# Optimization experiments

Hardware: AMD Instinct MI355X
Metric: run time of the kernel (lower is better)

Reference implementation:

```python
import jax, jax.numpy as jnp
import numpy as np

POSE, Z, H, E = 62, 32, 256, 6

def setup_inputs() -> dict:
    key = jax.random.key(0)
    ks = jax.random.split(key, 32)
    it = iter(ks)
    def W(o, i):
        return (jax.random.normal(next(it), (o, i), jnp.float32) * 0.05)
    def B(o):
        return jnp.zeros((o,), jnp.float32)
    def WE(o, i):
        return (jax.random.normal(next(it), (E, o, i), jnp.float32) * 0.05)
    def BE(o):
        return jnp.zeros((E, o), jnp.float32)
    d = {}
    d['prev_pose'] = jax.random.normal(next(it), (POSE,), jnp.float32)
    d['curr_pose'] = jax.random.normal(next(it), (POSE,), jnp.float32)
    d['eps'] = jax.random.normal(next(it), (Z,), jnp.float32)
    # encoder
    d['enc_w0'], d['enc_b0'] = W(H, POSE + POSE), B(H)
    d['enc_w1'], d['enc_b1'] = W(H, H), B(H)
    d['enc_w2'], d['enc_b2'] = W(H, H), B(H)
    d['mu_w'], d['mu_b'] = W(Z, H), B(Z)
    d['lv_w'], d['lv_b'] = W(Z, H), B(Z)
    # gating network
    d['gate_w0'], d['gate_b0'] = W(H, Z + POSE), B(H)
    d['gate_w1'], d['gate_b1'] = W(H, H), B(H)
    d['gate_w2'], d['gate_b2'] = W(H, H), B(H)
    d['gate_w3'], d['gate_b3'] = W(E, H), B(E)
    # 6 experts, stacked on leading expert axis
    d['exp_w0'], d['exp_b0'] = WE(H, Z + POSE), BE(H)
    d['exp_w1'], d['exp_b1'] = WE(H, Z + H), BE(H)
    d['exp_w2'], d['exp_b2'] = WE(H, Z + H), BE(H)
    d['exp_w3'], d['exp_b3'] = WE(POSE, Z + H), BE(POSE)
    return d

def _forward(prev_pose, curr_pose, eps,
             enc_w0, enc_b0, enc_w1, enc_b1, enc_w2, enc_b2,
             mu_w, mu_b, lv_w, lv_b,
             gate_w0, gate_b0, gate_w1, gate_b1, gate_w2, gate_b2,
             gate_w3, gate_b3,
             exp_w0, exp_b0, exp_w1, exp_b1, exp_w2, exp_b2,
             exp_w3, exp_b3):
    elu = jax.nn.elu
    # encode
    x = elu(enc_w0 @ jnp.concatenate([prev_pose, curr_pose]) + enc_b0)
    x = elu(enc_w1 @ x + enc_b1)
    x = elu(enc_w2 @ x + enc_b2)
    mu = mu_w @ x + mu_b
    logvar = lv_w @ x + lv_b
    # reparameterize (eps supplied as input for determinism)
    z = mu + eps * jnp.exp(0.5 * logvar)
    # gating network (raw logits, no softmax -- as in the original)
    g_in = jnp.concatenate([z, prev_pose])  # [94]
    g = elu(gate_w0 @ g_in + gate_b0)
    g = elu(gate_w1 @ g + gate_b1)
    g = elu(gate_w2 @ g + gate_b2)
    gates = gate_w3 @ g + gate_b3  # [6]
    # all 6 experts batched along leading axis e
    z_e = jnp.broadcast_to(z, (E, Z))  # [6,32]
    h = elu(jnp.einsum('eoh,h->eo', exp_w0, g_in) + exp_b0)       # [6,256]
    h = elu(jnp.einsum('eoh,eh->eo', exp_w1,
                       jnp.concatenate([z_e, h], axis=1)) + exp_b1)
    h = elu(jnp.einsum('eoh,eh->eo', exp_w2,
                       jnp.concatenate([z_e, h], axis=1)) + exp_b2)
    out_e = jnp.einsum('eoh,eh->eo', exp_w3,
                       jnp.concatenate([z_e, h], axis=1)) + exp_b3  # [6,62]
    decoded = jnp.sum(out_e * gates[:, None], axis=0)  # [62]
    return decoded, mu, logvar

def reference(prev_pose, curr_pose, eps,
              enc_w0, enc_b0, enc_w1, enc_b1, enc_w2, enc_b2,
              mu_w, mu_b, lv_w, lv_b,
              gate_w0, gate_b0, gate_w1, gate_b1, gate_w2, gate_b2,
              gate_w3, gate_b3,
              exp_w0, exp_b0, exp_w1, exp_b1, exp_w2, exp_b2,
              exp_w3, exp_b3):
    return _forward(prev_pose, curr_pose, eps,
                    enc_w0, enc_b0, enc_w1, enc_b1, enc_w2, enc_b2,
                    mu_w, mu_b, lv_w, lv_b,
                    gate_w0, gate_b0, gate_w1, gate_b1, gate_w2, gate_b2,
                    gate_w3, gate_b3,
                    exp_w0, exp_b0, exp_w1, exp_b1, exp_w2, exp_b2,
                    exp_w3, exp_b3)
```

## Files before the change

kernel.cpp:

```cpp
#include <hip/hip_runtime.h>
#include <math.h>


#define NWG    128
#define NWAVES (NWG * 4)
#define BLOCK  256
#define MAGIC  0x7E57A11E

__device__ __align__(128) float g_a0[256];
__device__ __align__(128) float g_a1[256];
__device__ __align__(128) float g_a2[256];
__device__ __align__(128) float g_mu[32];
__device__ __align__(128) float g_lv[32];
__device__ __align__(128) float g_g0[256];
__device__ __align__(128) float g_g1[256];
__device__ __align__(128) float g_g2[256];
__device__ __align__(128) float g_gates[32];
__device__ __align__(128) float g_h0[1536];
__device__ __align__(128) float g_h1[1536];
__device__ __align__(128) float g_h2[1536];
__device__ __align__(128) float g_oute[384];

struct P {
  const float *prev, *curr, *eps;
  const float *ew0,*eb0,*ew1,*eb1,*ew2,*eb2;
  const float *muw,*mub,*lvw,*lvb;
  const float *gw0,*gb0,*gw1,*gb1,*gw2,*gb2,*gw3,*gb3;
  const float *xw0,*xb0,*xw1,*xb1,*xw2,*xb2,*xw3,*xb3;
  float* out;
};

__device__ __forceinline__ float cload(const float* a) {
  int v = __hip_atomic_load((const int*)a, __ATOMIC_RELAXED,
                            __HIP_MEMORY_SCOPE_AGENT);
  return __int_as_float(v);
}
__device__ __forceinline__ void cstore(float* a, float v) {
  __hip_atomic_store((int*)a, __float_as_int(v), __ATOMIC_RELAXED,
                     __HIP_MEMORY_SCOPE_AGENT);
}
__device__ __forceinline__ float4 cload4(const float* a) {
  float4 r;
  r.x = cload(a + 0); r.y = cload(a + 1);
  r.z = cload(a + 2); r.w = cload(a + 3);
  return r;
}
__device__ __forceinline__ void gll16(const void* g, void* l) {
  __builtin_amdgcn_global_load_lds((const __attribute__((address_space(1))) void*)g,
                                   (__attribute__((address_space(3))) void*)l,
                                   16, 0, 0);
}
__device__ __forceinline__ void gll4(const void* g, void* l) {
  __builtin_amdgcn_global_load_lds((const __attribute__((address_space(1))) void*)g,
                                   (__attribute__((address_space(3))) void*)l,
                                   4, 0, 0);
}
__device__ __forceinline__ float wred(float v) {
#pragma unroll
  for (int m = 32; m; m >>= 1) v += __shfl_xor(v, m, 64);
  return v;
}
__device__ __forceinline__ float elu(float x) { return x > 0.f ? x : expm1f(x); }
__device__ __forceinline__ float dot4(float4 a, float4 b) {
  return a.x*b.x + a.y*b.y + a.z*b.z + a.w*b.w;
}

__device__ __forceinline__ int* slotp(int* flags, int ph, int wg) {
  return &flags[((ph - 1) * NWG + wg) * 16];
}
__device__ __forceinline__ void bar_arrive(int* flags, int ph) {
  __syncthreads();
  if (threadIdx.x == 0)
    __hip_atomic_store(slotp(flags, ph, blockIdx.x), MAGIC,
                       __ATOMIC_RELAXED, __HIP_MEMORY_SCOPE_AGENT);
}
__device__ __forceinline__ void bar_poll(int* flags, int ph, int nprod) {
  if (threadIdx.x < 64) {
    const int l = threadIdx.x;
    for (;;) {
      bool ok = true;
      for (int w = l; w < nprod; w += 64)
        ok &= (__hip_atomic_load(slotp(flags, ph, w),
                                 __ATOMIC_RELAXED, __HIP_MEMORY_SCOPE_AGENT)
               == MAGIC);
      if (ok) break;
      __builtin_amdgcn_s_sleep(2);
    }
  }
  __syncthreads();
}

__global__ __launch_bounds__(BLOCK, 1) void mvae_main(P p, int* flags) {
  const int tid  = threadIdx.x;
  const int lane = tid & 63;
  const int wvin = tid >> 6;
  const int Wv   = blockIdx.x * 4 + wvin;

  __shared__ __align__(16) float s_w1[4][256];
  __shared__ __align__(16) float s_w2[4][256];
  __shared__ __align__(16) float s_w3[4][256];
  __shared__ __align__(16) float s_w4[4][4][96];
  __shared__ __align__(16) float s_w5[4][4][288];
  __shared__ __align__(16) float s_w6[4][4][288];
  __shared__ __align__(16) float s_w7[4][288];
  __shared__ float s_o[384];
  __shared__ float s_gg[8];

  if (Wv < 256)
    gll16(p.ew1 + Wv * 256 + lane * 4, s_w1[wvin]);

  if (Wv < 256) {
    const float* wr = p.ew0 + Wv * 124;
    float wa = wr[lane];
    float wb = (lane < 60) ? wr[64 + lane] : 0.f;
    float xa = (lane < 62) ? p.prev[lane] : p.curr[lane - 62];
    float xb = (lane < 60) ? p.curr[lane + 2] : 0.f;
    float s = wred(wa * xa + wb * xb);
    if (!lane) cstore(&g_a0[Wv], elu(s + p.eb0[Wv]));
  }
  bar_arrive(flags, 1);
  if (Wv < 256)
    gll16(p.ew2 + Wv * 256 + lane * 4, s_w2[wvin]);
  if (Wv < 64) {
    const float* src = (Wv < 32) ? p.muw + Wv * 256 : p.lvw + (Wv - 32) * 256;
    gll16(src + lane * 4, s_w3[wvin]);
  }
  bar_poll(flags, 1, 64);

  if (Wv < 256) {
    float4 w = *(const float4*)(s_w1[wvin] + 4 * lane);
    float4 x = cload4(g_a0 + 4 * lane);
    float s = wred(dot4(w, x));
    if (!lane) cstore(&g_a1[Wv], elu(s + p.eb1[Wv]));
  }
  bar_arrive(flags, 2);
#pragma unroll
  for (int k = 0; k < 4; ++k) {
    int r = Wv + NWAVES * k;
    if (r < 1792) {
      const float* src = (r < 256) ? p.gw0 + r * 94 : p.xw0 + (size_t)(r - 256) * 94;
      float* dst = s_w4[wvin][k];
      if (lane < 23)       gll16(src + lane * 4, dst);
      else if (lane == 23) { gll4(src + 92, dst + 69);
                             gll4(src + 93, dst + 70); }
    }
  }
#pragma unroll
  for (int k = 0; k < 4; ++k) {
    int r = Wv + NWAVES * k;
    if (r < 1792) {
      float* dst = s_w5[wvin][k];
      if (r < 256) gll16(p.gw1 + r * 256 + lane * 4, dst);
      else {
        const float* src = p.xw1 + (size_t)(r - 256) * 288;
        gll16(src + lane * 4, dst);
        if (lane < 8) gll16(src + 256 + lane * 4, dst + 256);
      }
    }
  }
  bar_poll(flags, 2, 64);

  if (Wv < 256) {
    float4 w = *(const float4*)(s_w2[wvin] + 4 * lane);
    float4 x = cload4(g_a1 + 4 * lane);
    float s = wred(dot4(w, x));
    if (!lane) cstore(&g_a2[Wv], elu(s + p.eb2[Wv]));
  }
  bar_arrive(flags, 3);
#pragma unroll
  for (int k = 0; k < 4; ++k) {
    int r = Wv + NWAVES * k;
    if (r < 1792) {
      float* dst = s_w6[wvin][k];
      if (r < 256) gll16(p.gw2 + r * 256 + lane * 4, dst);
      else {
        const float* src = p.xw2 + (size_t)(r - 256) * 288;
        gll16(src + lane * 4, dst);
        if (lane < 8) gll16(src + 256 + lane * 4, dst + 256);
      }
    }
  }
  if (Wv < 6) {
    gll16(p.gw3 + Wv * 256 + lane * 4, s_w7[wvin]);
  } else if (Wv < 378) {
    const float* src = p.xw3 + (size_t)(Wv - 6) * 288;
    float* dst = s_w7[wvin];
    gll16(src + lane * 4, dst);
    if (lane < 8) gll16(src + 256 + lane * 4, dst + 256);
  }
  bar_poll(flags, 3, 64);

  if (Wv < 64) {
    float4 w = *(const float4*)(s_w3[wvin] + 4 * lane);
    float4 x = cload4(g_a2 + 4 * lane);
    float s = wred(dot4(w, x));
    if (!lane) {
      if (Wv < 32) { float v = s + p.mub[Wv]; cstore(&g_mu[Wv], v); p.out[62 + Wv] = v; }
      else { int r = Wv - 32; float v = s + p.lvb[r]; cstore(&g_lv[r], v); p.out[94 + r] = v; }
    }
  }
  bar_arrive(flags, 4);
  bar_poll(flags, 4, 16);

  float zs = 0.f;
  if (lane < 32)
    zs = cload(&g_mu[lane]) + p.eps[lane] * expf(0.5f * cload(&g_lv[lane]));
  float4 z4;
  z4.x = __shfl(zs, (4 * lane + 0) & 63, 64);
  z4.y = __shfl(zs, (4 * lane + 1) & 63, 64);
  z4.z = __shfl(zs, (4 * lane + 2) & 63, 64);
  z4.w = __shfl(zs, (4 * lane + 3) & 63, 64);
  float prevA = (lane >= 32 && lane < 94) ? p.prev[lane - 32] : 0.f;
  float prevB = (lane < 30) ? p.prev[32 + lane] : 0.f;
  float xa94 = (lane < 32) ? zs : prevA;

#pragma unroll
  for (int k = 0; k < 4; ++k) {
    int r = Wv + NWAVES * k;
    if (r < 1792) {
      const float* wrow = s_w4[wvin][k];
      float wa = wrow[lane];
      float wb = (lane < 30) ? wrow[64 + lane] : 0.f;
      float s = wred(wa * xa94 + wb * prevB);
      if (!lane) {
        if (r < 256) cstore(&g_g0[r], elu(s + p.gb0[r]));
        else         cstore(&g_h0[r - 256], elu(s + p.xb0[r - 256]));
      }
    }
  }
  bar_arrive(flags, 5);
  bar_poll(flags, 5, NWG);

#pragma unroll
  for (int k = 0; k < 4; ++k) {
    int r = Wv + NWAVES * k;
    if (r < 1792) {
      const float* wrow = s_w5[wvin][k];
      float4 w = *(const float4*)(wrow + 4 * lane);
      if (r < 256) {
        float4 x = cload4(g_g0 + 4 * lane);
        float s = wred(dot4(w, x));
        if (!lane) cstore(&g_g1[r], elu(s + p.gb1[r]));
      } else {
        int q = r - 256, e = q >> 8;
        const float* hsrc = g_h0 + e * 256;
        float4 xh = z4;
        if (lane >= 8) xh = cload4(hsrc + 4 * lane - 32);
        float s = dot4(w, xh);
        if (lane < 32) s += wrow[256 + lane] * cload(hsrc + 224 + lane);
        s = wred(s);
        if (!lane) cstore(&g_h1[q], elu(s + p.xb1[q]));
      }
    }
  }
  bar_arrive(flags, 6);
  bar_poll(flags, 6, NWG);

#pragma unroll
  for (int k = 0; k < 4; ++k) {
    int r = Wv + NWAVES * k;
    if (r < 1792) {
      const float* wrow = s_w6[wvin][k];
      float4 w = *(const float4*)(wrow + 4 * lane);
      if (r < 256) {
        float4 x = cload4(g_g1 + 4 * lane);
        float s = wred(dot4(w, x));
        if (!lane) cstore(&g_g2[r], elu(s + p.gb2[r]));
      } else {
        int q = r - 256, e = q >> 8;
        const float* hsrc = g_h1 + e * 256;
        float4 xh = z4;
        if (lane >= 8) xh = cload4(hsrc + 4 * lane - 32);
        float s = dot4(w, xh);
        if (lane < 32) s += wrow[256 + lane] * cload(hsrc + 224 + lane);
        s = wred(s);
        if (!lane) cstore(&g_h2[q], elu(s + p.xb2[q]));
      }
    }
  }
  bar_arrive(flags, 7);
  bar_poll(flags, 7, NWG);

  if (Wv < 6) {
    float4 w = *(const float4*)(s_w7[wvin] + 4 * lane);
    float4 x = cload4(g_g2 + 4 * lane);
    float s = wred(dot4(w, x));
    if (!lane) cstore(&g_gates[Wv], s + p.gb3[Wv]);
  } else if (Wv < 378) {
    int q = Wv - 6, e = q / 62;
    const float* wrow = s_w7[wvin];
    float4 w = *(const float4*)(wrow + 4 * lane);
    const float* hsrc = g_h2 + e * 256;
    float4 xh = z4;
    if (lane >= 8) xh = cload4(hsrc + 4 * lane - 32);
    float s = dot4(w, xh);
    if (lane < 32) s += wrow[256 + lane] * cload(hsrc + 224 + lane);
    s = wred(s);
    if (!lane) cstore(&g_oute[q], s + p.xb3[q]);
  }

  bar_arrive(flags, 8);
  if (blockIdx.x != 0) return;
  bar_poll(flags, 8, NWG);

  s_o[tid] = cload(&g_oute[tid]);
  if (tid < 116) s_o[tid + 256] = cload(&g_oute[tid + 256]);
  if (tid < 6)   s_gg[tid] = cload(&g_gates[tid]);
  __syncthreads();
  if (tid < 62) {
    float s = 0.f;
#pragma unroll
    for (int e = 0; e < 6; ++e) s += s_o[e * 62 + tid] * s_gg[e];
    p.out[tid] = s;
  }

  for (int idx = tid; idx < 8 * NWG; idx += BLOCK)
    __hip_atomic_store(&flags[idx * 16], 0,
                       __ATOMIC_RELAXED, __HIP_MEMORY_SCOPE_AGENT);
}

extern "C" void kernel_launch(void* const* d_in, const int* in_sizes, int n_in,
                              void* d_out, int out_size, void* d_ws, size_t ws_size,
                              hipStream_t stream) {
  (void)in_sizes; (void)n_in; (void)out_size; (void)ws_size;
  const float* const* in = (const float* const*)d_in;
  P p;
  p.prev = in[0];  p.curr = in[1];  p.eps = in[2];
  p.ew0 = in[3];   p.eb0 = in[4];   p.ew1 = in[5];  p.eb1 = in[6];
  p.ew2 = in[7];   p.eb2 = in[8];
  p.muw = in[9];   p.mub = in[10];  p.lvw = in[11]; p.lvb = in[12];
  p.gw0 = in[13];  p.gb0 = in[14];  p.gw1 = in[15]; p.gb1 = in[16];
  p.gw2 = in[17];  p.gb2 = in[18];  p.gw3 = in[19]; p.gb3 = in[20];
  p.xw0 = in[21];  p.xb0 = in[22];  p.xw1 = in[23]; p.xb1 = in[24];
  p.xw2 = in[25];  p.xb2 = in[26];  p.xw3 = in[27]; p.xb3 = in[28];
  p.out = (float*)d_out;

  int* flags = (int*)d_ws;
  mvae_main<<<NWG, BLOCK, 0, stream>>>(p, flags);
}
```

Measured before the change: 33.08 us.

## Compute mu/logvar redundantly per block to remove a grid barrier

Every block now loads all 64 mu/logvar weight rows into LDS and computes mu, logvar and z locally. This removes the grid-wide barrier phase that used to publish those values through global memory. Blocks outside the first 64 also skip polling phases 1 and 2, since they produce nothing for those phases, and the poll sleep interval is shortened. The cost is 64KB of extra LDS per block and redundant weight traffic and compute in all 128 blocks.

```diff
diff --git a/kernel.cpp b/kernel.cpp
--- a/kernel.cpp
+++ b/kernel.cpp
@@ -6,12 +6,11 @@
 #define NWAVES (NWG * 4)
 #define BLOCK  256
 #define MAGIC  0x7E57A11E
+#define NPHASE 7
 
 __device__ __align__(128) float g_a0[256];
 __device__ __align__(128) float g_a1[256];
 __device__ __align__(128) float g_a2[256];
-__device__ __align__(128) float g_mu[32];
-__device__ __align__(128) float g_lv[32];
 __device__ __align__(128) float g_g0[256];
 __device__ __align__(128) float g_g1[256];
 __device__ __align__(128) float g_g2[256];
@@ -84,7 +83,7 @@
                                  __ATOMIC_RELAXED, __HIP_MEMORY_SCOPE_AGENT)
                == MAGIC);
       if (ok) break;
-      __builtin_amdgcn_s_sleep(2);
+      __builtin_amdgcn_s_sleep(1);
     }
   }
   __syncthreads();
@@ -95,14 +94,17 @@
   const int lane = tid & 63;
   const int wvin = tid >> 6;
   const int Wv   = blockIdx.x * 4 + wvin;
+  const bool early = (blockIdx.x < 64);
 
   __shared__ __align__(16) float s_w1[4][256];
   __shared__ __align__(16) float s_w2[4][256];
-  __shared__ __align__(16) float s_w3[4][256];
+  __shared__ __align__(16) float s_wml[4][16 * 256];
   __shared__ __align__(16) float s_w4[4][4][96];
   __shared__ __align__(16) float s_w5[4][4][288];
   __shared__ __align__(16) float s_w6[4][4][288];
   __shared__ __align__(16) float s_w7[4][288];
+  __shared__ float s_ml[64];
+  __shared__ float s_z[32];
   __shared__ float s_o[384];
   __shared__ float s_gg[8];
 
@@ -121,11 +123,14 @@
   bar_arrive(flags, 1);
   if (Wv < 256)
     gll16(p.ew2 + Wv * 256 + lane * 4, s_w2[wvin]);
-  if (Wv < 64) {
-    const float* src = (Wv < 32) ? p.muw + Wv * 256 : p.lvw + (Wv - 32) * 256;
-    gll16(src + lane * 4, s_w3[wvin]);
-  }
-  bar_poll(flags, 1, 64);
+#pragma unroll
+  for (int i = 0; i < 16; ++i) {
+    int row = wvin * 16 + i;
+    const float* src = (row < 32) ? p.muw + row * 256
+                                  : p.lvw + (row - 32) * 256;
+    gll16(src + lane * 4, s_wml[wvin] + i * 256);
+  }
+  if (early) bar_poll(flags, 1, 64);
 
   if (Wv < 256) {
     float4 w = *(const float4*)(s_w1[wvin] + 4 * lane);
@@ -158,7 +163,7 @@
       }
     }
   }
-  bar_poll(flags, 2, 64);
+  if (early) bar_poll(flags, 2, 64);
 
   if (Wv < 256) {
     float4 w = *(const float4*)(s_w2[wvin] + 4 * lane);
@@ -190,29 +195,28 @@
   }
   bar_poll(flags, 3, 64);
 
-  if (Wv < 64) {
-    float4 w = *(const float4*)(s_w3[wvin] + 4 * lane);
+  {
     float4 x = cload4(g_a2 + 4 * lane);
-    float s = wred(dot4(w, x));
-    if (!lane) {
-      if (Wv < 32) { float v = s + p.mub[Wv]; cstore(&g_mu[Wv], v); p.out[62 + Wv] = v; }
-      else { int r = Wv - 32; float v = s + p.lvb[r]; cstore(&g_lv[r], v); p.out[94 + r] = v; }
-    }
-  }
-  bar_arrive(flags, 4);
-  bar_poll(flags, 4, 16);
-
-  float zs = 0.f;
-  if (lane < 32)
-    zs = cload(&g_mu[lane]) + p.eps[lane] * expf(0.5f * cload(&g_lv[lane]));
-  float4 z4;
-  z4.x = __shfl(zs, (4 * lane + 0) & 63, 64);
-  z4.y = __shfl(zs, (4 * lane + 1) & 63, 64);
-  z4.z = __shfl(zs, (4 * lane + 2) & 63, 64);
-  z4.w = __shfl(zs, (4 * lane + 3) & 63, 64);
+#pragma unroll
+    for (int i = 0; i < 16; ++i) {
+      float4 w = *(const float4*)(s_wml[wvin] + i * 256 + 4 * lane);
+      float s = wred(dot4(w, x));
+      int row = wvin * 16 + i;
+      if (!lane)
+        s_ml[row] = s + ((row < 32) ? p.mub[row] : p.lvb[row - 32]);
+    }
+  }
+  __syncthreads();
+  if (tid < 32) {
+    float mu = s_ml[tid], lv = s_ml[32 + tid];
+    s_z[tid] = mu + p.eps[tid] * expf(0.5f * lv);
+    if (blockIdx.x == 0) { p.out[62 + tid] = mu; p.out[94 + tid] = lv; }
+  }
+  __syncthreads();
+
   float prevA = (lane >= 32 && lane < 94) ? p.prev[lane - 32] : 0.f;
   float prevB = (lane < 30) ? p.prev[32 + lane] : 0.f;
-  float xa94 = (lane < 32) ? zs : prevA;
+  float xa94 = (lane < 32) ? s_z[lane] : prevA;
 
 #pragma unroll
   for (int k = 0; k < 4; ++k) {
@@ -228,8 +232,8 @@
       }
     }
   }
-  bar_arrive(flags, 5);
-  bar_poll(flags, 5, NWG);
+  bar_arrive(flags, 4);
+  bar_poll(flags, 4, NWG);
 
 #pragma unroll
   for (int k = 0; k < 4; ++k) {
@@ -244,8 +248,9 @@
       } else {
         int q = r - 256, e = q >> 8;
         const float* hsrc = g_h0 + e * 256;
-        float4 xh = z4;
-        if (lane >= 8) xh = cload4(hsrc + 4 * lane - 32);
+        float4 xh;
+        if (lane < 8) xh = *(const float4*)(s_z + 4 * lane);
+        else          xh = cload4(hsrc + 4 * lane - 32);
         float s = dot4(w, xh);
         if (lane < 32) s += wrow[256 + lane] * cload(hsrc + 224 + lane);
         s = wred(s);
@@ -253,8 +258,8 @@
       }
     }
   }
-  bar_arrive(flags, 6);
-  bar_poll(flags, 6, NWG);
+  bar_arrive(flags, 5);
+  bar_poll(flags, 5, NWG);
 
 #pragma unroll
   for (int k = 0; k < 4; ++k) {
@@ -269,8 +274,9 @@
       } else {
         int q = r - 256, e = q >> 8;
         const float* hsrc = g_h1 + e * 256;
-        float4 xh = z4;
-        if (lane >= 8) xh = cload4(hsrc + 4 * lane - 32);
+        float4 xh;
+        if (lane < 8) xh = *(const float4*)(s_z + 4 * lane);
+        else          xh = cload4(hsrc + 4 * lane - 32);
         float s = dot4(w, xh);
         if (lane < 32) s += wrow[256 + lane] * cload(hsrc + 224 + lane);
         s = wred(s);
@@ -278,8 +284,8 @@
       }
     }
   }
-  bar_arrive(flags, 7);
-  bar_poll(flags, 7, NWG);
+  bar_arrive(flags, 6);
+  bar_poll(flags, 6, NWG);
 
   if (Wv < 6) {
     float4 w = *(const float4*)(s_w7[wvin] + 4 * lane);
@@ -291,17 +297,18 @@
     const float* wrow = s_w7[wvin];
     float4 w = *(const float4*)(wrow + 4 * lane);
     const float* hsrc = g_h2 + e * 256;
-    float4 xh = z4;
-    if (lane >= 8) xh = cload4(hsrc + 4 * lane - 32);
+    float4 xh;
+    if (lane < 8) xh = *(const float4*)(s_z + 4 * lane);
+    else          xh = cload4(hsrc + 4 * lane - 32);
     float s = dot4(w, xh);
     if (lane < 32) s += wrow[256 + lane] * cload(hsrc + 224 + lane);
     s = wred(s);
     if (!lane) cstore(&g_oute[q], s + p.xb3[q]);
   }
 
-  bar_arrive(flags, 8);
+  bar_arrive(flags, 7);
   if (blockIdx.x != 0) return;
-  bar_poll(flags, 8, NWG);
+  bar_poll(flags, 7, NWG);
 
   s_o[tid] = cload(&g_oute[tid]);
   if (tid < 116) s_o[tid + 256] = cload(&g_oute[tid + 256]);
@@ -314,7 +321,7 @@
     p.out[tid] = s;
   }
 
-  for (int idx = tid; idx < 8 * NWG; idx += BLOCK)
+  for (int idx = tid; idx < NPHASE * NWG; idx += BLOCK)
     __hip_atomic_store(&flags[idx * 16], 0,
                        __ATOMIC_RELAXED, __HIP_MEMORY_SCOPE_AGENT);
 }
```

Result: slower. 38.59 us (+16.6%).
